# Optimization experiments

Hardware: AMD Instinct MI355X
Metric: run time of the kernel (lower is better)

Reference implementation:

```python
import jax, jax.numpy as jnp
import numpy as np

B, N, M, U, L = 2048, 256, 128, 512, 2   # batch, memory locations, memory width, num_units, num_layers
RH, WH, SH = 2, 2, 1                      # read heads, write heads, conv_shift_range
CLIP = 20.0
HEAD_R = M + 3 + (2 * SH + 1)             # 134 = k(M)+beta+g+s(2r+1)+gamma
HEAD_W = HEAD_R + 2 * M                   # 390 = + erase(M) + add(M)


def setup_inputs():
    key = jax.random.key(0)
    ks = jax.random.split(key, 12)
    def nrm(k, shape, s=0.05):
        return jax.random.normal(k, shape, jnp.float32) * s
    return {
        "X": jax.random.normal(ks[0], (B, U), jnp.float32),
        "m0": nrm(ks[1], (1, N, M), 0.5),
        "H0": nrm(ks[2], (L, 1, U)),
        "C0": nrm(ks[3], (L, 1, U)),
        "R0": nrm(ks[4], (RH, 1, M)),
        "A0": nrm(ks[5], (RH + WH, 1, N)),
        "W_prep": nrm(ks[6], (M * RH, U)),
        "b_prep": jnp.zeros((U,), jnp.float32),
        "W_lstm": nrm(ks[7], (L, 3 * U, 4 * U)),
        "b_lstm": jnp.zeros((L, 4 * U), jnp.float32),
        "W_r": nrm(ks[8], (U, RH * HEAD_R)),
        "b_r": jnp.zeros((RH * HEAD_R,), jnp.float32),
        "W_w": nrm(ks[9], (U, WH * HEAD_W)),
        "b_w": jnp.zeros((WH * HEAD_W,), jnp.float32),
        "W_ou": nrm(ks[10], (U + RH * M, U)),
        "b_ou": jnp.zeros((U,), jnp.float32),
    }


def _addressing(k, beta, g, s, gamma, m, a_prev):
    # k [B,M], beta/g/gamma [B], s [B,2*SH+1], m [B,N,M], a_prev [B,N]
    inner = jnp.einsum('bnm,bm->bn', m, k)
    k_norm = jnp.sqrt(jnp.sum(k * k, axis=1, keepdims=True))   # [B,1]
    m_norm = jnp.sqrt(jnp.sum(m * m, axis=2))                  # [B,N]
    K = inner / (k_norm * m_norm + 1e-8)
    w_c = jax.nn.softmax(beta[:, None] * K, axis=1)            # exp/sum in source == softmax
    w_g = g[:, None] * w_c + (1.0 - g[:, None]) * a_prev
    # The stacked-slice s_matrix in the source is exactly circular convolution:
    # w_conv[i] = sum_d s_d * w_g[(i - d) mod N], d in {0..SH, -SH..-1} matching s layout.
    shifts = list(range(0, SH + 1)) + list(range(-SH, 0))
    w_conv = sum(s[:, j:j + 1] * jnp.roll(w_g, shifts[j], axis=1) for j in range(2 * SH + 1))
    w_sharp = w_conv ** gamma[:, None]
    return w_sharp / jnp.sum(w_sharp, axis=1, keepdims=True)


def reference(X, m0, H0, C0, R0, A0, W_prep, b_prep, W_lstm, b_lstm,
              W_r, b_r, W_w, b_w, W_ou, b_ou):
    b = X.shape[0]
    m = jnp.broadcast_to(m0, (b, N, M))
    R_prev = [jnp.broadcast_to(jnp.tanh(R0[i]), (b, M)) for i in range(RH)]
    A_prev = [jnp.broadcast_to(jax.nn.softmax(A0[i], axis=-1), (b, N)) for i in range(RH + WH)]

    # controller
    h = jnp.concatenate(R_prev, axis=1) @ W_prep + b_prep
    for l in range(L):
        x_in = jnp.concatenate([X, h], axis=1)                              # [B,2U]
        h_prev = jnp.broadcast_to(H0[l], (b, U))
        c_prev = jnp.broadcast_to(C0[l], (b, U))
        z = jnp.concatenate([x_in, h_prev], axis=1) @ W_lstm[l] + b_lstm[l]  # [B,4U]
        i_g, f_g, g_g, o_g = jnp.split(z, 4, axis=1)
        c = jax.nn.sigmoid(f_g) * c_prev + jax.nn.sigmoid(i_g) * jnp.tanh(g_g)
        h = jax.nn.sigmoid(o_g) * jnp.tanh(c)
    h = jnp.clip(h, -CLIP, CLIP)

    r_heads = (h @ W_r + b_r).reshape(b, RH, HEAD_R)
    w_heads = (h @ W_w + b_w).reshape(b, WH, HEAD_W)
    heads = [r_heads[:, i] for i in range(RH)] + [w_heads[:, i] for i in range(WH)]

    A_t = []
    for ii, hd in enumerate(heads):
        A_t.append(_addressing(
            k=jnp.tanh(hd[:, :M]),
            beta=jax.nn.softplus(hd[:, M]),
            g=jax.nn.sigmoid(hd[:, M + 1]),
            s=jax.nn.softmax(hd[:, M + 2:M + 2 + 2 * SH + 1], axis=-1),
            gamma=jax.nn.softplus(hd[:, M + 2 + 2 * SH + 1]),
            m=m, a_prev=A_prev[ii]))

    # reads from old memory
    R_t = [jnp.einsum('bn,bnm->bm', A_t[i], m) for i in range(RH)]

    # sequential erase/add writes
    m_t = m
    for ii in range(WH):
        w = A_t[RH + ii][:, :, None]                                  # [B,N,1]
        del_v = jax.nn.sigmoid(w_heads[:, ii, -2 * M:-M])[:, None, :]  # [B,1,M]
        add_v = jnp.tanh(w_heads[:, ii, -M:])[:, None, :]
        m_t = m_t * (1.0 - w * del_v) + w * add_v

    y = jnp.clip(jnp.concatenate([h] + R_t, axis=1) @ W_ou + b_ou, -CLIP, CLIP)
    return y, m_t
```

## Files before the change

kernel.cpp:

```cpp
#include <hip/hip_runtime.h>
#include <math.h>

static constexpr int Bn = 2048;
static constexpr int Nn = 256;
static constexpr int Mn = 128;
static constexpr int Un = 512;

static constexpr size_t OFF_MNORM = 4608;
static constexpr size_t OFF_APREV = 4864;
static constexpr size_t OFF_BIASH = 5888;
static constexpr size_t OFF_KMAT  = 16384;
static constexpr size_t OFF_HEADS = OFF_KMAT + (size_t)8192 * 256;
static constexpr size_t OFF_AT    = OFF_HEADS + (size_t)2048 * 1048;
static constexpr size_t OFF_ERA   = OFF_AT + (size_t)2 * 2048 * 256;
static constexpr size_t OFF_ADD   = OFF_ERA + (size_t)2048 * 256;
static constexpr size_t OFF_XHB   = OFF_ADD + (size_t)2048 * 256;
static constexpr size_t OFF_HCAT  = OFF_XHB + 524288;
static constexpr size_t OFF_W0T   = OFF_HCAT + 524288;
static constexpr size_t OFF_W1T   = OFF_W0T + 524288;
static constexpr size_t OFF_WRWT  = OFF_W1T + 1048576;
static constexpr size_t OFF_WCOMB = OFF_WRWT + 294912;
static constexpr size_t OFF_WR2T  = OFF_WCOMB + 262144;
static constexpr size_t OFF_M0B   = OFF_WR2T + 65536;
static constexpr size_t OFF_ZPART = OFF_M0B + 16384 + 524288;

static constexpr int S_X0  = 0;
static constexpr int S_M0  = 512;
static constexpr int S_W0  = 528;
static constexpr int S_W1  = 1552;
static constexpr int S_WR  = 3600;
static constexpr int S_WW  = 3744;
static constexpr int S_WOU = 4144;
static constexpr int S_WR2 = 4400;
static constexpr int S_CA  = 4528;
static constexpr int S_ZC  = 4529;
static constexpr int S_END = 4657;

#define DEV __device__ __forceinline__

typedef __attribute__((ext_vector_type(8))) short bf16x8;
typedef __attribute__((ext_vector_type(4))) float f32x4;
typedef __attribute__((ext_vector_type(8))) unsigned short ushort8;
typedef unsigned int u32;

DEV float sigf(float x) { return 1.0f / (1.0f + expf(-x)); }
DEV float softplusf(float x) { return x > 20.0f ? x : log1pf(expf(x)); }
DEV unsigned short f2bf(float f) {
    unsigned u = __float_as_uint(f);
    u = (u + 0x7FFFu + ((u >> 16) & 1u)) >> 16;
    return (unsigned short)u;
}
DEV void gload16(const unsigned short* g, unsigned short* l) {
    __builtin_amdgcn_global_load_lds(
        (const __attribute__((address_space(1))) u32*)g,
        (__attribute__((address_space(3))) u32*)l, 16, 0, 0);
}

DEV float blk_reduce_max(float v, float* red) {
    int tid = threadIdx.x;
    red[tid] = v; __syncthreads();
    for (int s = (int)blockDim.x >> 1; s > 0; s >>= 1) {
        if (tid < s) red[tid] = fmaxf(red[tid], red[tid + s]);
        __syncthreads();
    }
    float r = red[0]; __syncthreads();
    return r;
}
DEV float blk_reduce_sum(float v, float* red) {
    int tid = threadIdx.x;
    red[tid] = v; __syncthreads();
    for (int s = (int)blockDim.x >> 1; s > 0; s >>= 1) {
        if (tid < s) red[tid] += red[tid + s];
        __syncthreads();
    }
    float r = red[0]; __syncthreads();
    return r;
}

#define GEMM_STAGE(buf, k0)                                                     \
    {                                                                           \
        _Pragma("unroll")                                                       \
        for (int q = 0; q < 2; ++q)                                             \
            gload16(A  + (size_t)(row0 + q * 32 + (tid >> 3)) * lda + (k0) + ke,\
                    &As[buf][q * 2048 + tid * 8]);                              \
        _Pragma("unroll")                                                       \
        for (int q = 0; q < 4; ++q)                                             \
            gload16(Wt + (size_t)(col0 + q * 32 + (tid >> 3)) * ldw + (k0) + ke,\
                    &Ws[buf][q * 2048 + tid * 8]);                              \
    }

#define GEMM_PROLOG                                                             \
    __shared__ __align__(16) unsigned short As[2][64 * 64];                     \
    __shared__ __align__(16) unsigned short Ws[2][128 * 64];                    \
    const int tid  = threadIdx.x;                                               \
    const int lane = tid & 63;                                                  \
    const int wave = tid >> 6;                                                  \
    const int wr = wave >> 1, wc = wave & 1;                                    \
    const int row0 = blockIdx.x * 64;                                           \
    const int col0 = blockIdx.y * 128;                                          \
    const int ke = ((tid & 7) * 8) ^ (((tid >> 3) & 7) << 3);                   \
    const int frow = lane & 15;                                                 \
    const int fko  = (lane >> 4) * 8;                                           \
    const int fxm  = (frow & 7) << 3;                                           \
    f32x4 acc[2][4];                                                            \
    _Pragma("unroll")                                                           \
    for (int i = 0; i < 2; ++i)                                                 \
        _Pragma("unroll")                                                       \
        for (int j = 0; j < 4; ++j) acc[i][j] = (f32x4){0.f, 0.f, 0.f, 0.f};

#define GEMM_FRAGS_AND_MFMA(Ab, Wb)                                             \
    {                                                                           \
        bf16x8 af[2][2], wf[2][4];                                              \
        _Pragma("unroll")                                                       \
        for (int kk = 0; kk < 2; ++kk) {                                        \
            _Pragma("unroll")                                                   \
            for (int i = 0; i < 2; ++i) {                                       \
                int fr = wr * 32 + i * 16 + frow;                               \
                af[kk][i] = *(const bf16x8*)&(Ab)[fr * 64 + ((kk * 32 + fko) ^ fxm)]; \
            }                                                                   \
            _Pragma("unroll")                                                   \
            for (int j = 0; j < 4; ++j) {                                       \
                int fr = wc * 64 + j * 16 + frow;                               \
                wf[kk][j] = *(const bf16x8*)&(Wb)[fr * 64 + ((kk * 32 + fko) ^ fxm)]; \
            }                                                                   \
        }                                                                       \
        __builtin_amdgcn_s_setprio(1);                                          \
        _Pragma("unroll")                                                       \
        for (int kk = 0; kk < 2; ++kk)                                          \
            _Pragma("unroll")                                                   \
            for (int i = 0; i < 2; ++i)                                         \
                _Pragma("unroll")                                               \
                for (int j = 0; j < 4; ++j)                                     \
                    acc[i][j] = __builtin_amdgcn_mfma_f32_16x16x32_bf16(        \
                        af[kk][i], wf[kk][j], acc[i][j], 0, 0, 0);              \
        __builtin_amdgcn_s_setprio(0);                                          \
    }

#define GEMM_MAINLOOP(Kr)                                                       \
    {                                                                           \
        const int nt = (Kr) >> 6;                                               \
        int cur = 0;                                                            \
        GEMM_STAGE(0, 0);                                                       \
        for (int t = 0; t < nt; ++t) {                                          \
            __syncthreads();                                                    \
            if (t + 1 < nt) GEMM_STAGE(cur ^ 1, (t + 1) * 64);                  \
            GEMM_FRAGS_AND_MFMA(As[cur], Ws[cur]);                              \
            cur ^= 1;                                                           \
        }                                                                       \
    }

__global__ __launch_bounds__(256) void gemm_bf16(
    const unsigned short* __restrict__ A, int lda,
    const unsigned short* __restrict__ Wt, int ldw,
    const float* __restrict__ bias,
    float* __restrict__ C, unsigned short* __restrict__ Cb, int ldc,
    int Nr, int Kr, int epi)
{
    GEMM_PROLOG
    GEMM_MAINLOOP(Kr)
    #pragma unroll
    for (int i = 0; i < 2; ++i) {
        int m0r = row0 + wr * 32 + i * 16 + (lane >> 4) * 4;
        #pragma unroll
        for (int j = 0; j < 4; ++j) {
            int n = col0 + wc * 64 + j * 16 + (lane & 15);
            if (n >= Nr) continue;
            float bv = bias ? bias[n] : 0.f;
            #pragma unroll
            for (int r = 0; r < 4; ++r) {
                float v = acc[i][j][r] + bv;
                if (epi == 1) v = fminf(fmaxf(v, -20.f), 20.f);
                if (epi == 2) Cb[(size_t)(m0r + r) * ldc + n] = f2bf(v);
                else          C [(size_t)(m0r + r) * ldc + n] = v;
            }
        }
    }
}

__global__ __launch_bounds__(256) void gemm_pfold(
    const unsigned short* __restrict__ WR2T,
    const unsigned short* __restrict__ M0B,
    unsigned short* __restrict__ WCOMB)
{
    const unsigned short* A  = WR2T + blockIdx.z * 128;
    const unsigned short* Wt = M0B;
    const int lda = 256, ldw = 128;
    unsigned short* Cb = WCOMB + 512 + blockIdx.z * 256;
    GEMM_PROLOG
    GEMM_MAINLOOP(128)
    #pragma unroll
    for (int i = 0; i < 2; ++i) {
        int m0r = row0 + wr * 32 + i * 16 + (lane >> 4) * 4;
        #pragma unroll
        for (int j = 0; j < 4; ++j) {
            int n = col0 + wc * 64 + j * 16 + (lane & 15);
            #pragma unroll
            for (int r = 0; r < 4; ++r)
                Cb[(size_t)(m0r + r) * 1024 + n] = f2bf(acc[i][j][r]);
        }
    }
}

__global__ __launch_bounds__(256) void gemm_lstm(
    const unsigned short* __restrict__ A, int lda,
    const unsigned short* __restrict__ Wt, int ldw,
    const float* __restrict__ zpart, const float* __restrict__ b_lstm,
    int z, const float* __restrict__ c0,
    unsigned short* __restrict__ hout, int ldh, int Kr, int doclip)
{
    GEMM_PROLOG
    GEMM_MAINLOOP(Kr)
    const int uu = lane & 15;
    const int q  = (col0 >> 6) + wc;
    const int uq = q * 16 + uu;
    const float c0v = c0[uq];
    float bg[4];
    #pragma unroll
    for (int g = 0; g < 4; ++g) {
        int j = g * 512 + q * 16 + uu;
        float a = b_lstm[z * 2048 + j];
        #pragma unroll
        for (int p = 0; p < 8; ++p)
            a += zpart[((size_t)z * 8 + p) * 2048 + j];
        bg[g] = a;
    }
    #pragma unroll
    for (int i = 0; i < 2; ++i) {
        int rbase = row0 + wr * 32 + i * 16 + (lane >> 4) * 4;
        #pragma unroll
        for (int r = 0; r < 4; ++r) {
            float ig = acc[i][0][r] + bg[0];
            float fg = acc[i][1][r] + bg[1];
            float gg = acc[i][2][r] + bg[2];
            float og = acc[i][3][r] + bg[3];
            float c = sigf(fg) * c0v + sigf(ig) * tanhf(gg);
            float h = sigf(og) * tanhf(c);
            if (doclip) h = fminf(fmaxf(h, -20.f), 20.f);
            hout[(size_t)(rbase + r) * ldh + uq] = f2bf(h);
        }
    }
}

__global__ __launch_bounds__(256) void gemm_kmat(
    const float* __restrict__ heads,
    const unsigned short* __restrict__ M0B,
    float* __restrict__ C)
{
    __shared__ __align__(16) unsigned short As[2][64 * 64];
    __shared__ __align__(16) unsigned short Ws[2][128 * 64];
    const int tid  = threadIdx.x;
    const int lane = tid & 63;
    const int wave = tid >> 6;
    const int wr = wave >> 1, wc = wave & 1;
    const int row0 = blockIdx.x * 64;
    const int col0 = blockIdx.y * 128;
    const int ke = ((tid & 7) * 8) ^ (((tid >> 3) & 7) << 3);
    const int frow = lane & 15;
    const int fko  = (lane >> 4) * 8;
    const int fxm  = (frow & 7) << 3;
    f32x4 acc[2][4];
    #pragma unroll
    for (int i = 0; i < 2; ++i)
        #pragma unroll
        for (int j = 0; j < 4; ++j) acc[i][j] = (f32x4){0.f, 0.f, 0.f, 0.f};

#define KMAT_STAGE(buf, k0)                                                     \
    {                                                                           \
        _Pragma("unroll")                                                       \
        for (int q = 0; q < 2; ++q) {                                           \
            int R = row0 + q * 32 + (tid >> 3);                                 \
            int b = R >> 2, ih = R & 3;                                         \
            int cb = (ih < 2) ? ih * 134 : 268 + (ih - 2) * 390;                \
            const float* hp = heads + (size_t)b * 1048 + cb + (k0) + ke;        \
            ushort8 o;                                                          \
            _Pragma("unroll")                                                   \
            for (int j = 0; j < 8; ++j) o[j] = f2bf(tanhf(hp[j]));              \
            *(ushort8*)&As[buf][q * 2048 + tid * 8] = o;                        \
        }                                                                       \
        _Pragma("unroll")                                                       \
        for (int q = 0; q < 4; ++q)                                             \
            gload16(M0B + (size_t)(col0 + q * 32 + (tid >> 3)) * 128 + (k0) + ke,\
                    &Ws[buf][q * 2048 + tid * 8]);                              \
    }

    int cur = 0;
    KMAT_STAGE(0, 0);
    for (int t = 0; t < 2; ++t) {
        __syncthreads();
        if (t == 0) KMAT_STAGE(1, 64);
        GEMM_FRAGS_AND_MFMA(As[cur], Ws[cur]);
        cur ^= 1;
    }
#undef KMAT_STAGE
    #pragma unroll
    for (int i = 0; i < 2; ++i) {
        int m0r = row0 + wr * 32 + i * 16 + (lane >> 4) * 4;
        #pragma unroll
        for (int j = 0; j < 4; ++j) {
            int n = col0 + wc * 64 + j * 16 + (lane & 15);
            #pragma unroll
            for (int r = 0; r < 4; ++r)
                C[(size_t)(m0r + r) * 256 + n] = acc[i][j][r];
        }
    }
}

DEV void dev_cvt8(const float* src, int lds, unsigned short* dst, int ldd,
                  int c8, int bloc, int tid)
{
    size_t idx = (size_t)bloc * 256 + tid;
    size_t r = idx / c8, c = (idx % c8) * 8;
    const float* s = src + r * lds + c;
    float4 v0 = *(const float4*)s;
    float4 v1 = *(const float4*)(s + 4);
    ushort8 o;
    o[0] = f2bf(v0.x); o[1] = f2bf(v0.y); o[2] = f2bf(v0.z); o[3] = f2bf(v0.w);
    o[4] = f2bf(v1.x); o[5] = f2bf(v1.y); o[6] = f2bf(v1.z); o[7] = f2bf(v1.w);
    *(ushort8*)(dst + r * ldd + c) = o;
}

DEV void dev_cvtT(const float* src, int R, int C, int lds,
                  unsigned short* dst, int ldd, int mode, int bx, int by,
                  int tid, float* t )
{
    const int x = tid & 31;
    for (int y = tid >> 5; y < 32; y += 8) {
        int r = by * 32 + y, c = bx * 32 + x;
        int scol = c;
        if (mode) scol = ((c >> 4) & 3) * 512 + (c >> 6) * 16 + (c & 15);
        t[y * 33 + x] = (r < R && c < C) ? src[(size_t)r * lds + scol] : 0.f;
    }
    __syncthreads();
    for (int y = tid >> 5; y < 32; y += 8) {
        int c = bx * 32 + y, r = by * 32 + x;
        if (c < C && r < R) dst[(size_t)c * ldd + r] = f2bf(t[x * 33 + y]);
    }
}

__global__ __launch_bounds__(256) void k_prep(
    const float* __restrict__ X, const float* __restrict__ m0,
    const float* __restrict__ H0, const float* __restrict__ R0,
    const float* __restrict__ A0, const float* __restrict__ W_prep,
    const float* __restrict__ b_prep, const float* __restrict__ W_lstm,
    const float* __restrict__ W_r, const float* __restrict__ b_r,
    const float* __restrict__ W_w, const float* __restrict__ b_w,
    const float* __restrict__ W_ou, float* __restrict__ ws)
{
    __shared__ float sh[32 * 33 + 64];
    const int bid = blockIdx.x, tid = threadIdx.x;
    unsigned short* XHB   = (unsigned short*)(ws + OFF_XHB);
    unsigned short* W0T   = (unsigned short*)(ws + OFF_W0T);
    unsigned short* W1T   = (unsigned short*)(ws + OFF_W1T);
    unsigned short* WRWT  = (unsigned short*)(ws + OFF_WRWT);
    unsigned short* WCOMB = (unsigned short*)(ws + OFF_WCOMB);
    unsigned short* WR2T  = (unsigned short*)(ws + OFF_WR2T);
    unsigned short* M0B   = (unsigned short*)(ws + OFF_M0B);

    if (bid < S_M0) {
        dev_cvt8(X, 512, XHB, 1024, 64, bid - S_X0, tid);
    } else if (bid < S_W0) {
        dev_cvt8(m0, 128, M0B, 128, 16, bid - S_M0, tid);
    } else if (bid < S_W1) {
        int s = bid - S_W0;
        dev_cvtT(W_lstm, 512, 2048, 2048, W0T, 512, 1, s & 63, s >> 6, tid, sh);
    } else if (bid < S_WR) {
        int s = bid - S_W1;
        dev_cvtT(W_lstm + (size_t)1536 * 2048, 1024, 2048, 2048, W1T, 1024, 1,
                 s & 63, s >> 6, tid, sh);
    } else if (bid < S_WW) {
        int s = bid - S_WR;
        dev_cvtT(W_r, 512, 268, 268, WRWT, 512, 0, s % 9, s / 9, tid, sh);
    } else if (bid < S_WOU) {
        int s = bid - S_WW;
        dev_cvtT(W_w, 512, 780, 780, WRWT + (size_t)268 * 512, 512, 0,
                 s % 25, s / 25, tid, sh);
    } else if (bid < S_WR2) {
        int s = bid - S_WOU;
        dev_cvtT(W_ou, 512, 512, 512, WCOMB, 1024, 0, s & 15, s >> 4, tid, sh);
    } else if (bid < S_CA) {
        int s = bid - S_WR2;
        dev_cvtT(W_ou + (size_t)512 * 512, 256, 512, 512, WR2T, 256, 0,
                 s & 15, s >> 4, tid, sh);
    } else if (bid < S_ZC) {
        float* red = sh;
        for (int i = 0; i < 4; ++i) {
            float v = A0[i * 256 + tid];
            float mx = blk_reduce_max(v, red);
            float e = expf(v - mx);
            float s = blk_reduce_sum(e, red);
            ws[OFF_APREV + i * 256 + tid] = e / s;
        }
        float acc = 0.f;
        for (int m = 0; m < 128; ++m) {
            float t = m0[(size_t)tid * 128 + m];
            acc = fmaf(t, t, acc);
        }
        ws[OFF_MNORM + tid] = sqrtf(acc);
        for (int j = tid; j < 1152; j += 256)
            ws[OFF_BIASH + j] = (j < 268) ? b_r[j] : (j < 1048 ? b_w[j - 268] : 0.f);
    } else {
        int sub = bid - S_ZC;
        int colb = sub & 7, up = (sub >> 3) & 7, z = sub >> 6;
        int j = colb * 256 + tid;
        float acc = 0.f;
        if (z == 0) {
            if (up < 4) {
                sh[256 + tid] = tanhf(R0[tid]);
                __syncthreads();
                if (tid < 128) {
                    int u = up * 128 + tid;
                    float a = b_prep[u];
                    for (int k = 0; k < 256; ++k)
                        a = fmaf(sh[256 + k], W_prep[(size_t)k * 512 + u], a);
                    sh[tid] = a;
                }
                __syncthreads();
                const int u0 = up * 128;
                #pragma unroll 4
                for (int t = 0; t < 128; ++t)
                    acc = fmaf(sh[t], W_lstm[(size_t)(512 + u0 + t) * 2048 + j], acc);
            } else {
                const int u0 = up * 128;
                #pragma unroll 4
                for (int t = 0; t < 128; ++t)
                    acc = fmaf(H0[u0 - 512 + t],
                               W_lstm[(size_t)(512 + u0 + t) * 2048 + j], acc);
            }
        } else {
            const int u0 = up * 64;
            const float* W1 = W_lstm + (size_t)1536 * 2048;
            #pragma unroll 4
            for (int t = 0; t < 64; ++t)
                acc = fmaf(H0[512 + u0 + t], W1[(size_t)(1024 + u0 + t) * 2048 + j], acc);
        }
        (ws + OFF_ZPART)[((size_t)z * 8 + up) * 2048 + j] = acc;
    }
}

__global__ __launch_bounds__(256) void k_addr(
    const float* __restrict__ heads, const float* __restrict__ kmat,
    const float* __restrict__ mnorm, const float* __restrict__ aprev,
    float* __restrict__ at, unsigned short* __restrict__ hcat,
    float* __restrict__ era, float* __restrict__ addv)
{
    __shared__ float red[256];
    __shared__ float wgs[256];
    __shared__ float sc[6];
    const int b = blockIdx.x, i = blockIdx.y, tid = threadIdx.x;
    const int cb = (i < 2) ? i * 134 : 268 + (i - 2) * 390;
    const float* hd = heads + (size_t)b * 1048 + cb;
    float kv = (tid < 128) ? tanhf(hd[tid]) : 0.f;
    float ksq = blk_reduce_sum(kv * kv, red);
    float kn = sqrtf(ksq);
    if (i >= 2 && tid < 128) {
        era [((size_t)b * 2 + (i - 2)) * 128 + tid] = sigf(hd[134 + tid]);
        addv[((size_t)b * 2 + (i - 2)) * 128 + tid] = tanhf(hd[262 + tid]);
    }
    if (tid == 0) {
        sc[0] = softplusf(hd[128]);
        sc[1] = sigf(hd[129]);
        float v0 = hd[130], v1 = hd[131], v2 = hd[132];
        float mx = fmaxf(v0, fmaxf(v1, v2));
        float e0 = expf(v0 - mx), e1 = expf(v1 - mx), e2 = expf(v2 - mx);
        float ssum = e0 + e1 + e2;
        sc[2] = e0 / ssum; sc[3] = e1 / ssum; sc[4] = e2 / ssum;
        sc[5] = softplusf(hd[133]);
    }
    __syncthreads();
    const float beta = sc[0], g = sc[1], s0 = sc[2], s1 = sc[3], s2 = sc[4],
                gamma = sc[5];
    float inner = kmat[((size_t)b * 4 + i) * 256 + tid];
    float K = inner / (kn * mnorm[tid] + 1e-8f);
    float x = beta * K;
    float mx = blk_reduce_max(x, red);
    float e = expf(x - mx);
    float se = blk_reduce_sum(e, red);
    float wc = e / se;
    float wg = g * wc + (1.f - g) * aprev[i * 256 + tid];
    wgs[tid] = wg;
    __syncthreads();
    float wconv = s0 * wg + s1 * wgs[(tid + 255) & 255] + s2 * wgs[(tid + 1) & 255];
    float wsh = powf(wconv, gamma);
    float ssum = blk_reduce_sum(wsh, red);
    float w = wsh / ssum;
    if (i < 2) hcat[(size_t)b * 1024 + 512 + i * 256 + tid] = f2bf(w);
    else       at[((size_t)(i - 2) * Bn + b) * 256 + tid] = w;
}

__global__ void k_mem(const float* __restrict__ m0, const float* __restrict__ at,
                      const float* __restrict__ era, const float* __restrict__ addv,
                      float* __restrict__ outm)
{
    const size_t total = (size_t)Bn * Nn * (Mn / 4);
    for (size_t idx = (size_t)blockIdx.x * blockDim.x + threadIdx.x;
         idx < total; idx += (size_t)gridDim.x * blockDim.x) {
        int mq = (int)(idx & 31);
        int n  = (int)((idx >> 5) & 255);
        int b  = (int)(idx >> 13);
        float4 t  = reinterpret_cast<const float4*>(m0)[n * 32 + mq];
        float w0 = at[((size_t)0 * Bn + b) * 256 + n];
        float w1 = at[((size_t)1 * Bn + b) * 256 + n];
        float4 e0 = reinterpret_cast<const float4*>(era) [((size_t)b * 2 + 0) * 32 + mq];
        float4 a0 = reinterpret_cast<const float4*>(addv)[((size_t)b * 2 + 0) * 32 + mq];
        float4 e1 = reinterpret_cast<const float4*>(era) [((size_t)b * 2 + 1) * 32 + mq];
        float4 a1 = reinterpret_cast<const float4*>(addv)[((size_t)b * 2 + 1) * 32 + mq];
#define UPD(c) { t.c = t.c * (1.f - w0 * e0.c) + w0 * a0.c; \
                 t.c = t.c * (1.f - w1 * e1.c) + w1 * a1.c; }
        UPD(x) UPD(y) UPD(z) UPD(w)
#undef UPD
        reinterpret_cast<float4*>(outm)[idx] = t;
    }
}

extern "C" void kernel_launch(void* const* d_in, const int* in_sizes, int n_in,
                              void* d_out, int out_size, void* d_ws, size_t ws_size,
                              hipStream_t stream)
{
    const float* X      = (const float*)d_in[0];
    const float* m0     = (const float*)d_in[1];
    const float* H0     = (const float*)d_in[2];
    const float* C0     = (const float*)d_in[3];
    const float* R0     = (const float*)d_in[4];
    const float* A0     = (const float*)d_in[5];
    const float* W_prep = (const float*)d_in[6];
    const float* b_prep = (const float*)d_in[7];
    const float* W_lstm = (const float*)d_in[8];
    const float* b_lstm = (const float*)d_in[9];
    const float* W_r    = (const float*)d_in[10];
    const float* b_r    = (const float*)d_in[11];
    const float* W_w    = (const float*)d_in[12];
    const float* b_w    = (const float*)d_in[13];
    const float* W_ou   = (const float*)d_in[14];
    const float* b_ou   = (const float*)d_in[15];
    float* ws  = (float*)d_ws;
    float* out = (float*)d_out;

    unsigned short* XHB   = (unsigned short*)(ws + OFF_XHB);
    unsigned short* HCAT  = (unsigned short*)(ws + OFF_HCAT);
    unsigned short* W0T   = (unsigned short*)(ws + OFF_W0T);
    unsigned short* W1T   = (unsigned short*)(ws + OFF_W1T);
    unsigned short* WRWT  = (unsigned short*)(ws + OFF_WRWT);
    unsigned short* WCOMB = (unsigned short*)(ws + OFF_WCOMB);
    unsigned short* WR2T  = (unsigned short*)(ws + OFF_WR2T);
    unsigned short* M0B   = (unsigned short*)(ws + OFF_M0B);

    k_prep<<<S_END, 256, 0, stream>>>(
        X, m0, H0, R0, A0, W_prep, b_prep, W_lstm, W_r, b_r, W_w, b_w, W_ou, ws);

    gemm_pfold<<<dim3(8, 2, 2), 256, 0, stream>>>(WR2T, M0B, WCOMB);

    gemm_lstm<<<dim3(32, 16), 256, 0, stream>>>(
        XHB, 1024, W0T, 512, ws + OFF_ZPART, b_lstm, 0, C0, XHB + 512, 1024, 512, 0);
    gemm_lstm<<<dim3(32, 16), 256, 0, stream>>>(
        XHB, 1024, W1T, 1024, ws + OFF_ZPART, b_lstm, 1, C0 + 512, HCAT, 1024, 1024, 1);

    gemm_bf16<<<dim3(32, 9), 256, 0, stream>>>(
        HCAT, 1024, WRWT, 512, ws + OFF_BIASH, ws + OFF_HEADS, nullptr, 1048, 1048, 512, 0);

    gemm_kmat<<<dim3(128, 2), 256, 0, stream>>>(
        ws + OFF_HEADS, M0B, ws + OFF_KMAT);

    k_addr<<<dim3(Bn, 4), 256, 0, stream>>>(
        ws + OFF_HEADS, ws + OFF_KMAT, ws + OFF_MNORM, ws + OFF_APREV,
        ws + OFF_AT, HCAT, ws + OFF_ERA, ws + OFF_ADD);

    gemm_bf16<<<dim3(32, 4), 256, 0, stream>>>(
        HCAT, 1024, WCOMB, 1024, b_ou, out, nullptr, 512, 512, 1024, 1);

    k_mem<<<2048, 256, 0, stream>>>(
        m0, ws + OFF_AT, ws + OFF_ERA, ws + OFF_ADD, out + (size_t)Bn * Un);
}
```

Before: 205.7 us.

## Fuse pfold into layer-0 LSTM GEMM, tile memory update, and use wave-shuffle reductions

```diff
diff --git a/kernel.cpp b/kernel.cpp
--- a/kernel.cpp
+++ b/kernel.cpp
@@ -77,6 +77,35 @@
     return r;
 }
 
+DEV float wv_sum(float v) {
+    #pragma unroll
+    for (int off = 32; off; off >>= 1) v += __shfl_xor(v, off);
+    return v;
+}
+DEV float wv_max(float v) {
+    #pragma unroll
+    for (int off = 32; off; off >>= 1) v = fmaxf(v, __shfl_xor(v, off));
+    return v;
+}
+DEV float blk_sum4(float v, float* red4) {
+    v = wv_sum(v);
+    int w = threadIdx.x >> 6;
+    if ((threadIdx.x & 63) == 0) red4[w] = v;
+    __syncthreads();
+    float r = red4[0] + red4[1] + red4[2] + red4[3];
+    __syncthreads();
+    return r;
+}
+DEV float blk_max4(float v, float* red4) {
+    v = wv_max(v);
+    int w = threadIdx.x >> 6;
+    if ((threadIdx.x & 63) == 0) red4[w] = v;
+    __syncthreads();
+    float r = fmaxf(fmaxf(red4[0], red4[1]), fmaxf(red4[2], red4[3]));
+    __syncthreads();
+    return r;
+}
+
 #define GEMM_STAGE(buf, k0)                                                     \
     {                                                                           \
         _Pragma("unroll")                                                       \
@@ -89,15 +118,13 @@
                     &Ws[buf][q * 2048 + tid * 8]);                              \
     }
 
-#define GEMM_PROLOG                                                             \
+#define GEMM_PROLOG_CORE                                                        \
     __shared__ __align__(16) unsigned short As[2][64 * 64];                     \
     __shared__ __align__(16) unsigned short Ws[2][128 * 64];                    \
     const int tid  = threadIdx.x;                                               \
     const int lane = tid & 63;                                                  \
     const int wave = tid >> 6;                                                  \
     const int wr = wave >> 1, wc = wave & 1;                                    \
-    const int row0 = blockIdx.x * 64;                                           \
-    const int col0 = blockIdx.y * 128;                                          \
     const int ke = ((tid & 7) * 8) ^ (((tid >> 3) & 7) << 3);                   \
     const int frow = lane & 15;                                                 \
     const int fko  = (lane >> 4) * 8;                                           \
@@ -107,6 +134,11 @@
     for (int i = 0; i < 2; ++i)                                                 \
         _Pragma("unroll")                                                       \
         for (int j = 0; j < 4; ++j) acc[i][j] = (f32x4){0.f, 0.f, 0.f, 0.f};
+
+#define GEMM_PROLOG                                                             \
+    GEMM_PROLOG_CORE                                                            \
+    const int row0 = blockIdx.x * 64;                                           \
+    const int col0 = blockIdx.y * 128;
 
 #define GEMM_FRAGS_AND_MFMA(Ab, Wb)                                             \
     {                                                                           \
@@ -142,9 +174,18 @@
         int cur = 0;                                                            \
         GEMM_STAGE(0, 0);                                                       \
         for (int t = 0; t < nt; ++t) {                                          \
-            __syncthreads();                                                    \
-            if (t + 1 < nt) GEMM_STAGE(cur ^ 1, (t + 1) * 64);                  \
+            if (t + 1 < nt) {                                                   \
+                GEMM_STAGE(cur ^ 1, (t + 1) * 64);                              \
+                asm volatile("s_waitcnt vmcnt(6)" ::: "memory");                \
+            } else {                                                            \
+                asm volatile("s_waitcnt vmcnt(0)" ::: "memory");                \
+            }                                                                   \
+            __builtin_amdgcn_sched_barrier(0);                                  \
+            __builtin_amdgcn_s_barrier();                                       \
+            __builtin_amdgcn_sched_barrier(0);                                  \
             GEMM_FRAGS_AND_MFMA(As[cur], Ws[cur]);                              \
+            __builtin_amdgcn_sched_barrier(0);                                  \
+            __builtin_amdgcn_s_barrier();                                       \
             cur ^= 1;                                                           \
         }                                                                       \
     }
@@ -177,30 +218,6 @@
     }
 }
 
-__global__ __launch_bounds__(256) void gemm_pfold(
-    const unsigned short* __restrict__ WR2T,
-    const unsigned short* __restrict__ M0B,
-    unsigned short* __restrict__ WCOMB)
-{
-    const unsigned short* A  = WR2T + blockIdx.z * 128;
-    const unsigned short* Wt = M0B;
-    const int lda = 256, ldw = 128;
-    unsigned short* Cb = WCOMB + 512 + blockIdx.z * 256;
-    GEMM_PROLOG
-    GEMM_MAINLOOP(128)
-    #pragma unroll
-    for (int i = 0; i < 2; ++i) {
-        int m0r = row0 + wr * 32 + i * 16 + (lane >> 4) * 4;
-        #pragma unroll
-        for (int j = 0; j < 4; ++j) {
-            int n = col0 + wc * 64 + j * 16 + (lane & 15);
-            #pragma unroll
-            for (int r = 0; r < 4; ++r)
-                Cb[(size_t)(m0r + r) * 1024 + n] = f2bf(acc[i][j][r]);
-        }
-    }
-}
-
 __global__ __launch_bounds__(256) void gemm_lstm(
     const unsigned short* __restrict__ A, int lda,
     const unsigned short* __restrict__ Wt, int ldw,
@@ -241,28 +258,82 @@
     }
 }
 
+__global__ __launch_bounds__(256) void gemm_l0p(
+    const unsigned short* __restrict__ XHB,
+    const unsigned short* __restrict__ W0T,
+    const unsigned short* __restrict__ WR2T,
+    const unsigned short* __restrict__ M0B,
+    const float* __restrict__ zpart, const float* __restrict__ b_lstm,
+    const float* __restrict__ c0, unsigned short* __restrict__ hout,
+    unsigned short* __restrict__ WCOMB)
+{
+    const int by = blockIdx.y, bx = blockIdx.x;
+    const unsigned short *A, *Wt;
+    int lda, ldw, row0, col0, Kr;
+    unsigned short* pCb = nullptr;
+    if (by < 16) {
+        A = XHB;  lda = 1024; Wt = W0T; ldw = 512;
+        row0 = bx * 64; col0 = by * 128; Kr = 512;
+    } else {
+        int pz = bx >> 4, py = (bx >> 3) & 1, px = bx & 7;
+        A = WR2T + pz * 128; lda = 256; Wt = M0B; ldw = 128;
+        row0 = px * 64; col0 = py * 128; Kr = 128;
+        pCb = WCOMB + 512 + pz * 256;
+    }
+    GEMM_PROLOG_CORE
+    GEMM_MAINLOOP(Kr)
+    if (by < 16) {
+        const int uu = lane & 15;
+        const int q  = (col0 >> 6) + wc;
+        const int uq = q * 16 + uu;
+        const float c0v = c0[uq];
+        float bg[4];
+        #pragma unroll
+        for (int g = 0; g < 4; ++g) {
+            int j = g * 512 + q * 16 + uu;
+            float a = b_lstm[j];
+            #pragma unroll
+            for (int p = 0; p < 8; ++p)
+                a += zpart[(size_t)p * 2048 + j];
+            bg[g] = a;
+        }
+        #pragma unroll
+        for (int i = 0; i < 2; ++i) {
+            int rbase = row0 + wr * 32 + i * 16 + (lane >> 4) * 4;
+            #pragma unroll
+            for (int r = 0; r < 4; ++r) {
+                float ig = acc[i][0][r] + bg[0];
+                float fg = acc[i][1][r] + bg[1];
+                float gg = acc[i][2][r] + bg[2];
+                float og = acc[i][3][r] + bg[3];
+                float c = sigf(fg) * c0v + sigf(ig) * tanhf(gg);
+                float h = sigf(og) * tanhf(c);
+                hout[(size_t)(rbase + r) * 1024 + uq] = f2bf(h);
+            }
+        }
+    } else {
+        #pragma unroll
+        for (int i = 0; i < 2; ++i) {
+            int m0r = row0 + wr * 32 + i * 16 + (lane >> 4) * 4;
+            #pragma unroll
+            for (int j = 0; j < 4; ++j) {
+                int n = col0 + wc * 64 + j * 16 + (lane & 15);
+                #pragma unroll
+                for (int r = 0; r < 4; ++r)
+                    pCb[(size_t)(m0r + r) * 1024 + n] = f2bf(acc[i][j][r]);
+            }
+        }
+    }
+}
+
 __global__ __launch_bounds__(256) void gemm_kmat(
     const float* __restrict__ heads,
     const unsigned short* __restrict__ M0B,
     float* __restrict__ C)
 {
-    __shared__ __align__(16) unsigned short As[2][64 * 64];
-    __shared__ __align__(16) unsigned short Ws[2][128 * 64];
-    const int tid  = threadIdx.x;
-    const int lane = tid & 63;
-    const int wave = tid >> 6;
-    const int wr = wave >> 1, wc = wave & 1;
+    GEMM_PROLOG_CORE
     const int row0 = blockIdx.x * 64;
     const int col0 = blockIdx.y * 128;
-    const int ke = ((tid & 7) * 8) ^ (((tid >> 3) & 7) << 3);
-    const int frow = lane & 15;
-    const int fko  = (lane >> 4) * 8;
-    const int fxm  = (frow & 7) << 3;
-    f32x4 acc[2][4];
-    #pragma unroll
-    for (int i = 0; i < 2; ++i)
-        #pragma unroll
-        for (int j = 0; j < 4; ++j) acc[i][j] = (f32x4){0.f, 0.f, 0.f, 0.f};
 
 #define KMAT_STAGE(buf, k0)                                                     \
     {                                                                           \
@@ -443,15 +514,14 @@
     float* __restrict__ at, unsigned short* __restrict__ hcat,
     float* __restrict__ era, float* __restrict__ addv)
 {
-    __shared__ float red[256];
+    __shared__ float red4[4];
     __shared__ float wgs[256];
     __shared__ float sc[6];
     const int b = blockIdx.x, i = blockIdx.y, tid = threadIdx.x;
     const int cb = (i < 2) ? i * 134 : 268 + (i - 2) * 390;
     const float* hd = heads + (size_t)b * 1048 + cb;
     float kv = (tid < 128) ? tanhf(hd[tid]) : 0.f;
-    float ksq = blk_reduce_sum(kv * kv, red);
-    float kn = sqrtf(ksq);
+    float kn = sqrtf(blk_sum4(kv * kv, red4));
     if (i >= 2 && tid < 128) {
         era [((size_t)b * 2 + (i - 2)) * 128 + tid] = sigf(hd[134 + tid]);
         addv[((size_t)b * 2 + (i - 2)) * 128 + tid] = tanhf(hd[262 + tid]);
@@ -472,43 +542,69 @@
     float inner = kmat[((size_t)b * 4 + i) * 256 + tid];
     float K = inner / (kn * mnorm[tid] + 1e-8f);
     float x = beta * K;
-    float mx = blk_reduce_max(x, red);
+    float mx = blk_max4(x, red4);
     float e = expf(x - mx);
-    float se = blk_reduce_sum(e, red);
+    float se = blk_sum4(e, red4);
     float wc = e / se;
     float wg = g * wc + (1.f - g) * aprev[i * 256 + tid];
     wgs[tid] = wg;
     __syncthreads();
     float wconv = s0 * wg + s1 * wgs[(tid + 255) & 255] + s2 * wgs[(tid + 1) & 255];
     float wsh = powf(wconv, gamma);
-    float ssum = blk_reduce_sum(wsh, red);
+    float ssum = blk_sum4(wsh, red4);
     float w = wsh / ssum;
     if (i < 2) hcat[(size_t)b * 1024 + 512 + i * 256 + tid] = f2bf(w);
     else       at[((size_t)(i - 2) * Bn + b) * 256 + tid] = w;
 }
 
-__global__ void k_mem(const float* __restrict__ m0, const float* __restrict__ at,
-                      const float* __restrict__ era, const float* __restrict__ addv,
-                      float* __restrict__ outm)
-{
-    const size_t total = (size_t)Bn * Nn * (Mn / 4);
-    for (size_t idx = (size_t)blockIdx.x * blockDim.x + threadIdx.x;
-         idx < total; idx += (size_t)gridDim.x * blockDim.x) {
-        int mq = (int)(idx & 31);
-        int n  = (int)((idx >> 5) & 255);
-        int b  = (int)(idx >> 13);
-        float4 t  = reinterpret_cast<const float4*>(m0)[n * 32 + mq];
-        float w0 = at[((size_t)0 * Bn + b) * 256 + n];
-        float w1 = at[((size_t)1 * Bn + b) * 256 + n];
-        float4 e0 = reinterpret_cast<const float4*>(era) [((size_t)b * 2 + 0) * 32 + mq];
-        float4 a0 = reinterpret_cast<const float4*>(addv)[((size_t)b * 2 + 0) * 32 + mq];
-        float4 e1 = reinterpret_cast<const float4*>(era) [((size_t)b * 2 + 1) * 32 + mq];
-        float4 a1 = reinterpret_cast<const float4*>(addv)[((size_t)b * 2 + 1) * 32 + mq];
+__global__ __launch_bounds__(512) void k_memt(
+    const float* __restrict__ m0, const float* __restrict__ at,
+    const float* __restrict__ era, const float* __restrict__ addv,
+    float* __restrict__ outm)
+{
+    __shared__ __align__(16) float at_s[2][8][256];
+    __shared__ __align__(16) float er_s[2][8][128];
+    __shared__ __align__(16) float ad_s[2][8][128];
+    const int tid = threadIdx.x;
+    const int b0 = blockIdx.x * 8;
+    for (int t = tid; t < 1024; t += 512) {
+        int i = t >> 9, rem = t & 511;
+        int bb = rem >> 6, n4 = rem & 63;
+        ((float4*)&at_s[i][bb][0])[n4] =
+            ((const float4*)(at + ((size_t)i * Bn + b0 + bb) * 256))[n4];
+    }
+    {
+        int t = tid;
+        if (t < 512) {
+            int i = t >> 8, rem = t & 255;
+            int bb = rem >> 5, m4 = rem & 31;
+            ((float4*)&er_s[i][bb][0])[m4] =
+                ((const float4*)(era + ((size_t)(b0 + bb) * 2 + i) * 128))[m4];
+            ((float4*)&ad_s[i][bb][0])[m4] =
+                ((const float4*)(addv + ((size_t)(b0 + bb) * 2 + i) * 128))[m4];
+        }
+    }
+    __syncthreads();
+    const float4* m0v = (const float4*)m0;
+    float4* outv = (float4*)outm;
+    for (int pos = tid; pos < 8192; pos += 512) {
+        int mq = pos & 31, n = pos >> 5;
+        float4 t0 = m0v[pos];
+        #pragma unroll
+        for (int bb = 0; bb < 8; ++bb) {
+            float w0 = at_s[0][bb][n], w1 = at_s[1][bb][n];
+            float4 e0 = *(const float4*)&er_s[0][bb][mq * 4];
+            float4 a0 = *(const float4*)&ad_s[0][bb][mq * 4];
+            float4 e1 = *(const float4*)&er_s[1][bb][mq * 4];
+            float4 a1 = *(const float4*)&ad_s[1][bb][mq * 4];
+            float4 t = t0;
 #define UPD(c) { t.c = t.c * (1.f - w0 * e0.c) + w0 * a0.c; \
                  t.c = t.c * (1.f - w1 * e1.c) + w1 * a1.c; }
-        UPD(x) UPD(y) UPD(z) UPD(w)
+            UPD(x) UPD(y) UPD(z) UPD(w)
 #undef UPD
-        reinterpret_cast<float4*>(outm)[idx] = t;
+            __builtin_nontemporal_store(*(f32x4*)&t,
+                (f32x4*)&outv[(size_t)(b0 + bb) * 8192 + pos]);
+        }
     }
 }
 
@@ -547,10 +643,9 @@
     k_prep<<<S_END, 256, 0, stream>>>(
         X, m0, H0, R0, A0, W_prep, b_prep, W_lstm, W_r, b_r, W_w, b_w, W_ou, ws);
 
-    gemm_pfold<<<dim3(8, 2, 2), 256, 0, stream>>>(WR2T, M0B, WCOMB);
-
-    gemm_lstm<<<dim3(32, 16), 256, 0, stream>>>(
-        XHB, 1024, W0T, 512, ws + OFF_ZPART, b_lstm, 0, C0, XHB + 512, 1024, 512, 0);
+    gemm_l0p<<<dim3(32, 17), 256, 0, stream>>>(
+        XHB, W0T, WR2T, M0B, ws + OFF_ZPART, b_lstm, C0, XHB + 512, WCOMB);
+
     gemm_lstm<<<dim3(32, 16), 256, 0, stream>>>(
         XHB, 1024, W1T, 1024, ws + OFF_ZPART, b_lstm, 1, C0 + 512, HCAT, 1024, 1024, 1);
 
@@ -567,6 +662,6 @@
     gemm_bf16<<<dim3(32, 4), 256, 0, stream>>>(
         HCAT, 1024, WCOMB, 1024, b_ou, out, nullptr, 512, 512, 1024, 1);
 
-    k_mem<<<2048, 256, 0, stream>>>(
+    k_memt<<<256, 512, 0, stream>>>(
         m0, ws + OFF_AT, ws + OFF_ERA, ws + OFF_ADD, out + (size_t)Bn * Un);
 }
```

New measurement: 185.3 us. 1.11x faster.
